# Kernel tuning notes

Measured on AMD Instinct MI355X. Metric: run time of the kernel, lower is better.

## Reference

```python
import jax, jax.numpy as jnp
import numpy as np

N_HEAD = 4
D_MODEL = 256
FEAT_DIM = 256
D_K = D_MODEL // N_HEAD  # 64
TEMP = float(np.sqrt(D_K))
LN_EPS = 1e-5


def setup_inputs() -> dict:
    key = jax.random.key(0)
    ks = jax.random.split(key, 12)
    B, N_src, N_ngh = 2048, 1, 128
    src = jax.random.normal(ks[0], (B, N_src, FEAT_DIM), dtype=jnp.float32)
    seq = jax.random.normal(ks[1], (B, N_ngh, FEAT_DIM), dtype=jnp.float32)
    mask = jax.random.randint(ks[2], (B, N_ngh), 0, 2) > 0
    s_qk = np.sqrt(2.0 / (D_MODEL + D_K))
    w_qs = jax.random.normal(ks[3], (N_HEAD * D_K, D_MODEL), dtype=jnp.float32) * s_qk
    w_ks = jax.random.normal(ks[4], (N_HEAD * D_K, D_MODEL), dtype=jnp.float32) * s_qk
    w_vs = jax.random.normal(ks[5], (N_HEAD * D_K, D_MODEL), dtype=jnp.float32) * s_qk
    fc_w = jax.random.normal(ks[6], (D_MODEL, N_HEAD * D_K), dtype=jnp.float32) * 0.05
    fc_b = jnp.zeros((D_MODEL,), dtype=jnp.float32)
    ln_g = jnp.ones((D_MODEL,), dtype=jnp.float32)
    ln_b = jnp.zeros((D_MODEL,), dtype=jnp.float32)
    fc1_w = jax.random.normal(ks[7], (FEAT_DIM, 2 * D_MODEL), dtype=jnp.float32) * 0.05
    fc1_b = jnp.zeros((FEAT_DIM,), dtype=jnp.float32)
    fc2_w = jax.random.normal(ks[8], (FEAT_DIM, FEAT_DIM), dtype=jnp.float32) * 0.05
    fc2_b = jnp.zeros((FEAT_DIM,), dtype=jnp.float32)
    return {"src": src, "seq": seq, "mask": mask, "w_qs": w_qs, "w_ks": w_ks,
            "w_vs": w_vs, "fc_w": fc_w, "fc_b": fc_b, "ln_g": ln_g, "ln_b": ln_b,
            "fc1_w": fc1_w, "fc1_b": fc1_b, "fc2_w": fc2_w, "fc2_b": fc2_b}


def _forward(src, seq, mask, w_qs, w_ks, w_vs, fc_w, fc_b, ln_g, ln_b,
             fc1_w, fc1_b, fc2_w, fc2_b):
    B, N_src, _ = src.shape
    N_ngh = seq.shape[1]
    nn_ = N_ngh // N_src
    # projections (dropout is identity in eval mode)
    qh = (src @ w_qs.T).reshape(B, N_src, N_HEAD, D_K)              # bshd
    kh = (seq @ w_ks.T).reshape(B, N_src, nn_, N_HEAD, D_K)        # bsnhd
    vh = (seq @ w_vs.T).reshape(B, N_src, nn_, N_HEAD, D_K)
    scores = jnp.einsum('bshd,bsnhd->bshn', qh, kh) / TEMP          # [B,Ns,H,nn]
    # Replicate original mask layout exactly: attn rows are flat in (b,s,h)
    # order, but mask was built with .repeat(n_head,1,1) -> head-major tiling.
    flat = scores.reshape(B * N_src * N_HEAD, nn_)
    mask_rep = jnp.tile(mask.reshape(B * N_src, nn_), (N_HEAD, 1))  # [H*B*Ns, nn]
    flat = jnp.where(mask_rep, -1e10, flat)
    attn = jax.nn.softmax(flat, axis=-1).reshape(B, N_src, N_HEAD, nn_)
    out = jnp.einsum('bshn,bsnhd->bshd', attn, vh).reshape(B, N_src, N_HEAD * D_K)
    out = out @ fc_w.T + fc_b
    x = out + src  # residual (q == src since pos_dim == 0)
    mu = jnp.mean(x, axis=-1, keepdims=True)
    var = jnp.mean(jnp.square(x - mu), axis=-1, keepdims=True)
    x = (x - mu) * jax.lax.rsqrt(var + LN_EPS) * ln_g + ln_b
    # MergeLayer (non_linear=True)
    h = jax.nn.relu(jnp.concatenate([x, src], axis=-1) @ fc1_w.T + fc1_b)
    z = h @ fc2_w.T + fc2_b                                        # [B,Ns,feat]
    return z, attn


def reference(src, seq, mask, w_qs, w_ks, w_vs, fc_w, fc_b, ln_g, ln_b,
              fc1_w, fc1_b, fc2_w, fc2_b):
    return _forward(src, seq, mask, w_qs, w_ks, w_vs, fc_w, fc_b, ln_g, ln_b,
                    fc1_w, fc1_b, fc2_w, fc2_b)
```

## Files before the change

kernel.cpp:

```cpp
#include <hip/hip_runtime.h>

typedef unsigned int uint32;
typedef unsigned short ushort16;

#define DI __device__ __forceinline__

#define BATCH 2048
#define NN    128
#define DM    256
#define NH    4
#define DK    64

DI float bf2f(ushort16 h) { return __uint_as_float(((uint32)h) << 16); }

DI ushort16 f2bf(float f) {
    uint32 u = __float_as_uint(f);
    uint32 r = u + 0x7fffu + ((u >> 16) & 1u);
    return (ushort16)(r >> 16);
}

DI void unpack8(const uint4 v, float f[8]) {
    f[0] = __uint_as_float(v.x << 16);
    f[1] = __uint_as_float(v.x & 0xffff0000u);
    f[2] = __uint_as_float(v.y << 16);
    f[3] = __uint_as_float(v.y & 0xffff0000u);
    f[4] = __uint_as_float(v.z << 16);
    f[5] = __uint_as_float(v.z & 0xffff0000u);
    f[6] = __uint_as_float(v.w << 16);
    f[7] = __uint_as_float(v.w & 0xffff0000u);
}

DI float dot8(const float* a, const float f[8], float acc) {
    acc = fmaf(a[0], f[0], acc);
    acc = fmaf(a[1], f[1], acc);
    acc = fmaf(a[2], f[2], acc);
    acc = fmaf(a[3], f[3], acc);
    acc = fmaf(a[4], f[4], acc);
    acc = fmaf(a[5], f[5], acc);
    acc = fmaf(a[6], f[6], acc);
    acc = fmaf(a[7], f[7], acc);
    return acc;
}

#define WOFF_QS  0
#define WOFF_KS  65536
#define WOFF_VS  131072
#define WOFF_FC  196608
#define WOFF_FC1 262144
#define WOFF_FC2 393216

__global__ __launch_bounds__(256) void prep_kernel(
    const float* __restrict__ wqs, const float* __restrict__ wks,
    const float* __restrict__ wvs, const float* __restrict__ fcw,
    const float* __restrict__ fc1w, const float* __restrict__ fc2w,
    ushort16* __restrict__ out)
{
    const int bid = blockIdx.x;
    const float* srcp; size_t soff, doff;
    if (bid < 64)       { srcp = wqs;  soff = (size_t)bid * 1024;         doff = WOFF_QS;  }
    else if (bid < 128) { srcp = wks;  soff = (size_t)(bid - 64) * 1024;  doff = WOFF_KS;  }
    else if (bid < 192) { srcp = wvs;  soff = (size_t)(bid - 128) * 1024; doff = WOFF_VS;  }
    else if (bid < 256) { srcp = fcw;  soff = (size_t)(bid - 192) * 1024; doff = WOFF_FC;  }
    else if (bid < 384) { srcp = fc1w; soff = (size_t)(bid - 256) * 1024; doff = WOFF_FC1; }
    else                { srcp = fc2w; soff = (size_t)(bid - 384) * 1024; doff = WOFF_FC2; }
    const int t = threadIdx.x;
    float4 v = *(const float4*)(srcp + soff + t * 4);
    uint2 pk;
    pk.x = (uint32)f2bf(v.x) | ((uint32)f2bf(v.y) << 16);
    pk.y = (uint32)f2bf(v.z) | ((uint32)f2bf(v.w) << 16);
    *(uint2*)(out + doff + soff + t * 4) = pk;
}

__global__ __launch_bounds__(256) void qu_kernel(
    const float* __restrict__ src, const ushort16* __restrict__ wbf,
    float* __restrict__ u)
{
    __shared__ float sS[8][DM];
    __shared__ float sQ[8][DM];
    const int t  = threadIdx.x;
    const int b0 = blockIdx.x * 8;

    #pragma unroll
    for (int r = 0; r < 8; ++r) sS[r][t] = src[(size_t)(b0 + r) * DM + t];
    __syncthreads();

    {
        float acc[8] = {0.f,0.f,0.f,0.f,0.f,0.f,0.f,0.f};
        const ushort16* wrow = wbf + WOFF_QS + (size_t)t * DM;
        for (int kc = 0; kc < DM; kc += 8) {
            uint4 w8 = *(const uint4*)(wrow + kc);
            float wf[8]; unpack8(w8, wf);
            #pragma unroll
            for (int r = 0; r < 8; ++r) acc[r] = dot8(&sS[r][kc], wf, acc[r]);
        }
        #pragma unroll
        for (int r = 0; r < 8; ++r) sQ[r][t] = acc[r];
    }
    __syncthreads();

    const ushort16* wks = wbf + WOFF_KS;
    for (int h = 0; h < NH; ++h) {
        float ua[8] = {0.f,0.f,0.f,0.f,0.f,0.f,0.f,0.f};
        for (int dc = 0; dc < DK; dc += 8) {
            float wv[8];
            #pragma unroll
            for (int e = 0; e < 8; ++e)
                wv[e] = bf2f(wks[(size_t)(h * DK + dc + e) * DM + t]);
            #pragma unroll
            for (int r = 0; r < 8; ++r) {
                float4 qa = *(const float4*)&sQ[r][h * DK + dc];
                float4 qb = *(const float4*)&sQ[r][h * DK + dc + 4];
                float a = ua[r];
                a = fmaf(qa.x, wv[0], a); a = fmaf(qa.y, wv[1], a);
                a = fmaf(qa.z, wv[2], a); a = fmaf(qa.w, wv[3], a);
                a = fmaf(qb.x, wv[4], a); a = fmaf(qb.y, wv[5], a);
                a = fmaf(qb.z, wv[6], a); a = fmaf(qb.w, wv[7], a);
                ua[r] = a;
            }
        }
        #pragma unroll
        for (int r = 0; r < 8; ++r)
            u[(size_t)(b0 + r) * (NH * DM) + h * DM + t] = ua[r] * 0.125f;
    }
}

#define SEQ_STRIDE 264
#define U_STRIDE   264

__global__ __launch_bounds__(256) void attn_kernel(
    const float* __restrict__ seq, const int* __restrict__ mask,
    const float* __restrict__ u, float* __restrict__ c,
    float* __restrict__ attn_out)
{
    __shared__ ushort16 sseq[NN * SEQ_STRIDE];
    __shared__ float    sbuf[2048];
    __shared__ float    sattn[NN * NH];

    const int t = threadIdx.x;
    const int b = blockIdx.x;

    #pragma unroll
    for (int i = 0; i < 4; ++i)
        sbuf[i * U_STRIDE + t] = u[(size_t)b * 1024 + i * 256 + t];

    const float* sp = seq + (size_t)b * (NN * DM);
    #pragma unroll
    for (int it = 0; it < 32; ++it) {
        int idx = it * 1024 + t * 4;
        int row = idx >> 8, col = idx & 255;
        float4 v = *(const float4*)(sp + idx);
        uint2 pk;
        pk.x = (uint32)f2bf(v.x) | ((uint32)f2bf(v.y) << 16);
        pk.y = (uint32)f2bf(v.z) | ((uint32)f2bf(v.w) << 16);
        *(uint2*)&sseq[row * SEQ_STRIDE + col] = pk;
    }
    __syncthreads();

    {
        const int h  = t & 3;
        const int n0 = t >> 2;
        const float* uh = &sbuf[h * U_STRIDE];
        const ushort16* r0 = &sseq[n0 * SEQ_STRIDE];
        const ushort16* r1 = &sseq[(n0 + 64) * SEQ_STRIDE];
        float s0 = 0.f, s1 = 0.f;
        for (int kc = 0; kc < DM; kc += 8) {
            uint4 va = *(const uint4*)(r0 + kc);
            uint4 vb = *(const uint4*)(r1 + kc);
            float fa[8], fb[8];
            unpack8(va, fa); unpack8(vb, fb);
            s0 = dot8(&uh[kc], fa, s0);
            s1 = dot8(&uh[kc], fb, s1);
        }
        int mr = (4 * b + h) & (BATCH - 1);
        if (mask[(size_t)mr * NN + n0] != 0)      s0 = -1e10f;
        if (mask[(size_t)mr * NN + n0 + 64] != 0) s1 = -1e10f;
        sattn[n0 * 4 + h]        = s0;
        sattn[(n0 + 64) * 4 + h] = s1;
    }
    __syncthreads();

    {
        const int w = t >> 6, l = t & 63;
        float x0 = sattn[l * 4 + w], x1 = sattn[(l + 64) * 4 + w];
        float mx = fmaxf(x0, x1);
        #pragma unroll
        for (int o = 32; o > 0; o >>= 1) mx = fmaxf(mx, __shfl_xor(mx, o, 64));
        float e0 = __expf(x0 - mx), e1 = __expf(x1 - mx);
        float sm = e0 + e1;
        #pragma unroll
        for (int o = 32; o > 0; o >>= 1) sm += __shfl_xor(sm, o, 64);
        float inv = 1.f / sm;
        float a0 = e0 * inv, a1 = e1 * inv;
        sattn[l * 4 + w]        = a0;
        sattn[(l + 64) * 4 + w] = a1;
        attn_out[(size_t)b * (NH * NN) + w * NN + l]      = a0;
        attn_out[(size_t)b * (NH * NN) + w * NN + l + 64] = a1;
    }
    __syncthreads();

    {
        const int ng = t >> 7;
        const int jp = t & 127;
        float cc[4][2] = {{0.f,0.f},{0.f,0.f},{0.f,0.f},{0.f,0.f}};
        for (int i = 0; i < 64; ++i) {
            int n = ng * 64 + i;
            uint32 v = *(const uint32*)&sseq[n * SEQ_STRIDE + jp * 2];
            float f0 = __uint_as_float(v << 16);
            float f1 = __uint_as_float(v & 0xffff0000u);
            float4 at = *(const float4*)&sattn[n * 4];
            cc[0][0] = fmaf(at.x, f0, cc[0][0]); cc[0][1] = fmaf(at.x, f1, cc[0][1]);
            cc[1][0] = fmaf(at.y, f0, cc[1][0]); cc[1][1] = fmaf(at.y, f1, cc[1][1]);
            cc[2][0] = fmaf(at.z, f0, cc[2][0]); cc[2][1] = fmaf(at.z, f1, cc[2][1]);
            cc[3][0] = fmaf(at.w, f0, cc[3][0]); cc[3][1] = fmaf(at.w, f1, cc[3][1]);
        }
        __syncthreads();
        #pragma unroll
        for (int h = 0; h < 4; ++h) {
            sbuf[ng * 1024 + h * 256 + jp * 2]     = cc[h][0];
            sbuf[ng * 1024 + h * 256 + jp * 2 + 1] = cc[h][1];
        }
    }
    __syncthreads();
    #pragma unroll
    for (int h = 0; h < 4; ++h)
        c[(size_t)b * 1024 + h * 256 + t] = sbuf[h * 256 + t] + sbuf[1024 + h * 256 + t];
}

__global__ __launch_bounds__(256) void mlp_kernel(
    const float* __restrict__ c, const float* __restrict__ src,
    const ushort16* __restrict__ wbf,
    const float* __restrict__ fcb, const float* __restrict__ lng,
    const float* __restrict__ lnb, const float* __restrict__ fc1b,
    const float* __restrict__ fc2b, float* __restrict__ zout)
{
    __shared__ float sC[8][1024];
    __shared__ float sA[8][256];
    __shared__ float sX[8][256];
    __shared__ float sS[8][256];
    __shared__ float sH[8][256];
    __shared__ float sRed[4][8][2];

    const int t  = threadIdx.x;
    const int b0 = blockIdx.x * 8;
    const int h  = t >> 6;

    #pragma unroll
    for (int i = 0; i < 8; ++i)
        *(float4*)&sC[i][t * 4] = *(const float4*)&c[(size_t)(b0 + i) * 1024 + t * 4];
    #pragma unroll
    for (int r = 0; r < 8; ++r) sS[r][t] = src[(size_t)(b0 + r) * DM + t];
    __syncthreads();

    {
        float acc[8] = {0.f,0.f,0.f,0.f,0.f,0.f,0.f,0.f};
        const ushort16* wr = wbf + WOFF_VS + (size_t)t * DM;
        for (int kc = 0; kc < DM; kc += 8) {
            uint4 w8 = *(const uint4*)(wr + kc);
            float wf[8]; unpack8(w8, wf);
            #pragma unroll
            for (int r = 0; r < 8; ++r) acc[r] = dot8(&sC[r][h * 256 + kc], wf, acc[r]);
        }
        #pragma unroll
        for (int r = 0; r < 8; ++r) sA[r][t] = acc[r];
    }
    __syncthreads();

    float xv[8];
    {
        float acc[8] = {0.f,0.f,0.f,0.f,0.f,0.f,0.f,0.f};
        const ushort16* wr = wbf + WOFF_FC + (size_t)t * DM;
        for (int kc = 0; kc < DM; kc += 8) {
            uint4 w8 = *(const uint4*)(wr + kc);
            float wf[8]; unpack8(w8, wf);
            #pragma unroll
            for (int r = 0; r < 8; ++r) acc[r] = dot8(&sA[r][kc], wf, acc[r]);
        }
        float bb = fcb[t];
        #pragma unroll
        for (int r = 0; r < 8; ++r) xv[r] = acc[r] + bb + sS[r][t];
    }
    {
        const int w = t >> 6, l = t & 63;
        #pragma unroll
        for (int r = 0; r < 8; ++r) {
            float vs = xv[r], vq = xv[r] * xv[r];
            #pragma unroll
            for (int o = 32; o > 0; o >>= 1) {
                vs += __shfl_xor(vs, o, 64);
                vq += __shfl_xor(vq, o, 64);
            }
            if (l == 0) { sRed[w][r][0] = vs; sRed[w][r][1] = vq; }
        }
        __syncthreads();
        float g = lng[t], bb = lnb[t];
        #pragma unroll
        for (int r = 0; r < 8; ++r) {
            float S = sRed[0][r][0] + sRed[1][r][0] + sRed[2][r][0] + sRed[3][r][0];
            float Q = sRed[0][r][1] + sRed[1][r][1] + sRed[2][r][1] + sRed[3][r][1];
            float mu  = S * (1.f / 256.f);
            float var = Q * (1.f / 256.f) - mu * mu;
            float rs  = rsqrtf(var + 1e-5f);
            sX[r][t] = (xv[r] - mu) * rs * g + bb;
        }
    }
    __syncthreads();

    {
        float acc[8] = {0.f,0.f,0.f,0.f,0.f,0.f,0.f,0.f};
        const ushort16* wr = wbf + WOFF_FC1 + (size_t)t * 512;
        for (int kc = 0; kc < 256; kc += 8) {
            uint4 w8 = *(const uint4*)(wr + kc);
            float wf[8]; unpack8(w8, wf);
            #pragma unroll
            for (int r = 0; r < 8; ++r) acc[r] = dot8(&sX[r][kc], wf, acc[r]);
        }
        for (int kc = 0; kc < 256; kc += 8) {
            uint4 w8 = *(const uint4*)(wr + 256 + kc);
            float wf[8]; unpack8(w8, wf);
            #pragma unroll
            for (int r = 0; r < 8; ++r) acc[r] = dot8(&sS[r][kc], wf, acc[r]);
        }
        float bb = fc1b[t];
        #pragma unroll
        for (int r = 0; r < 8; ++r) sH[r][t] = fmaxf(acc[r] + bb, 0.f);
    }
    __syncthreads();

    {
        float acc[8] = {0.f,0.f,0.f,0.f,0.f,0.f,0.f,0.f};
        const ushort16* wr = wbf + WOFF_FC2 + (size_t)t * DM;
        for (int kc = 0; kc < DM; kc += 8) {
            uint4 w8 = *(const uint4*)(wr + kc);
            float wf[8]; unpack8(w8, wf);
            #pragma unroll
            for (int r = 0; r < 8; ++r) acc[r] = dot8(&sH[r][kc], wf, acc[r]);
        }
        float bb = fc2b[t];
        #pragma unroll
        for (int r = 0; r < 8; ++r)
            zout[(size_t)(b0 + r) * DM + t] = acc[r] + bb;
    }
}

extern "C" void kernel_launch(void* const* d_in, const int* in_sizes, int n_in,
                              void* d_out, int out_size, void* d_ws, size_t ws_size,
                              hipStream_t stream)
{
    const float* src  = (const float*)d_in[0];
    const float* seq  = (const float*)d_in[1];
    const int*   mask = (const int*)d_in[2];
    const float* wqs  = (const float*)d_in[3];
    const float* wks  = (const float*)d_in[4];
    const float* wvs  = (const float*)d_in[5];
    const float* fcw  = (const float*)d_in[6];
    const float* fcb  = (const float*)d_in[7];
    const float* lng  = (const float*)d_in[8];
    const float* lnb  = (const float*)d_in[9];
    const float* fc1w = (const float*)d_in[10];
    const float* fc1b = (const float*)d_in[11];
    const float* fc2w = (const float*)d_in[12];
    const float* fc2b = (const float*)d_in[13];

    float* zout     = (float*)d_out;
    float* attn_out = zout + (size_t)BATCH * DM;

    float* u = (float*)d_ws;
    float* cbuf = u + (size_t)BATCH * 1024;
    ushort16* wbf = (ushort16*)(cbuf + (size_t)BATCH * 1024);

    prep_kernel<<<448, 256, 0, stream>>>(wqs, wks, wvs, fcw, fc1w, fc2w, wbf);
    qu_kernel<<<256, 256, 0, stream>>>(src, wbf, u);
    attn_kernel<<<BATCH, 256, 0, stream>>>(seq, mask, u, cbuf, attn_out);
    mlp_kernel<<<256, 256, 0, stream>>>(cbuf, src, wbf, fcb, lng, lnb,
                                        fc1b, fc2b, zout);
}
```

Measured before the change: 471.9 us.

## Fuse query projection and key-folding into attention kernel, drop qu_kernel

Removes the separate qu_kernel and computes q = src·Wq and u = q·Wk (scaled) per batch row inside the attention kernel, right after the seq tile is staged. This eliminates one launch and the global round trip of the u buffer. In exchange, each attention block re-reads the full bf16 Wq and Wk weights (about 256 KB per block) instead of amortising them over 8 rows, which adds L2 traffic and per-block latency.

```diff
diff --git a/kernel.cpp b/kernel.cpp
--- a/kernel.cpp
+++ b/kernel.cpp
@@ -71,77 +71,24 @@
     *(uint2*)(out + doff + soff + t * 4) = pk;
 }
 
-__global__ __launch_bounds__(256) void qu_kernel(
-    const float* __restrict__ src, const ushort16* __restrict__ wbf,
-    float* __restrict__ u)
-{
-    __shared__ float sS[8][DM];
-    __shared__ float sQ[8][DM];
-    const int t  = threadIdx.x;
-    const int b0 = blockIdx.x * 8;
-
-    #pragma unroll
-    for (int r = 0; r < 8; ++r) sS[r][t] = src[(size_t)(b0 + r) * DM + t];
-    __syncthreads();
-
-    {
-        float acc[8] = {0.f,0.f,0.f,0.f,0.f,0.f,0.f,0.f};
-        const ushort16* wrow = wbf + WOFF_QS + (size_t)t * DM;
-        for (int kc = 0; kc < DM; kc += 8) {
-            uint4 w8 = *(const uint4*)(wrow + kc);
-            float wf[8]; unpack8(w8, wf);
-            #pragma unroll
-            for (int r = 0; r < 8; ++r) acc[r] = dot8(&sS[r][kc], wf, acc[r]);
-        }
-        #pragma unroll
-        for (int r = 0; r < 8; ++r) sQ[r][t] = acc[r];
-    }
-    __syncthreads();
-
-    const ushort16* wks = wbf + WOFF_KS;
-    for (int h = 0; h < NH; ++h) {
-        float ua[8] = {0.f,0.f,0.f,0.f,0.f,0.f,0.f,0.f};
-        for (int dc = 0; dc < DK; dc += 8) {
-            float wv[8];
-            #pragma unroll
-            for (int e = 0; e < 8; ++e)
-                wv[e] = bf2f(wks[(size_t)(h * DK + dc + e) * DM + t]);
-            #pragma unroll
-            for (int r = 0; r < 8; ++r) {
-                float4 qa = *(const float4*)&sQ[r][h * DK + dc];
-                float4 qb = *(const float4*)&sQ[r][h * DK + dc + 4];
-                float a = ua[r];
-                a = fmaf(qa.x, wv[0], a); a = fmaf(qa.y, wv[1], a);
-                a = fmaf(qa.z, wv[2], a); a = fmaf(qa.w, wv[3], a);
-                a = fmaf(qb.x, wv[4], a); a = fmaf(qb.y, wv[5], a);
-                a = fmaf(qb.z, wv[6], a); a = fmaf(qb.w, wv[7], a);
-                ua[r] = a;
-            }
-        }
-        #pragma unroll
-        for (int r = 0; r < 8; ++r)
-            u[(size_t)(b0 + r) * (NH * DM) + h * DM + t] = ua[r] * 0.125f;
-    }
-}
-
 #define SEQ_STRIDE 264
 #define U_STRIDE   264
 
 __global__ __launch_bounds__(256) void attn_kernel(
-    const float* __restrict__ seq, const int* __restrict__ mask,
-    const float* __restrict__ u, float* __restrict__ c,
-    float* __restrict__ attn_out)
+    const float* __restrict__ src, const float* __restrict__ seq,
+    const int* __restrict__ mask, const ushort16* __restrict__ wbf,
+    float* __restrict__ c, float* __restrict__ attn_out)
 {
     __shared__ ushort16 sseq[NN * SEQ_STRIDE];
     __shared__ float    sbuf[2048];
     __shared__ float    sattn[NN * NH];
+    __shared__ float    ssrc[DM];
+    __shared__ float    sQ[DM];
 
     const int t = threadIdx.x;
     const int b = blockIdx.x;
 
-    #pragma unroll
-    for (int i = 0; i < 4; ++i)
-        sbuf[i * U_STRIDE + t] = u[(size_t)b * 1024 + i * 256 + t];
+    ssrc[t] = src[(size_t)b * DM + t];
 
     const float* sp = seq + (size_t)b * (NN * DM);
     #pragma unroll
@@ -153,6 +100,39 @@
         pk.x = (uint32)f2bf(v.x) | ((uint32)f2bf(v.y) << 16);
         pk.y = (uint32)f2bf(v.z) | ((uint32)f2bf(v.w) << 16);
         *(uint2*)&sseq[row * SEQ_STRIDE + col] = pk;
+    }
+    __syncthreads();
+
+    {
+        float acc = 0.f;
+        const ushort16* wrow = wbf + WOFF_QS + (size_t)t * DM;
+        for (int kc = 0; kc < DM; kc += 8) {
+            uint4 w8 = *(const uint4*)(wrow + kc);
+            float wf[8]; unpack8(w8, wf);
+            acc = dot8(&ssrc[kc], wf, acc);
+        }
+        sQ[t] = acc * 0.125f;
+    }
+    __syncthreads();
+
+    {
+        const int w = t >> 6, l = t & 63;
+        float u00 = 0.f, u01 = 0.f, u10 = 0.f, u11 = 0.f;
+        const ushort16* wk = wbf + WOFF_KS + (size_t)w * DK * DM;
+        #pragma unroll 8
+        for (int d = 0; d < DK; ++d) {
+            float qd = sQ[w * DK + d];
+            uint32 va = *(const uint32*)(wk + d * DM + 2 * l);
+            uint32 vb = *(const uint32*)(wk + d * DM + 128 + 2 * l);
+            u00 = fmaf(qd, __uint_as_float(va << 16), u00);
+            u01 = fmaf(qd, __uint_as_float(va & 0xffff0000u), u01);
+            u10 = fmaf(qd, __uint_as_float(vb << 16), u10);
+            u11 = fmaf(qd, __uint_as_float(vb & 0xffff0000u), u11);
+        }
+        sbuf[w * U_STRIDE + 2 * l]           = u00;
+        sbuf[w * U_STRIDE + 2 * l + 1]       = u01;
+        sbuf[w * U_STRIDE + 128 + 2 * l]     = u10;
+        sbuf[w * U_STRIDE + 128 + 2 * l + 1] = u11;
     }
     __syncthreads();
 
@@ -364,13 +344,11 @@
     float* zout     = (float*)d_out;
     float* attn_out = zout + (size_t)BATCH * DM;
 
-    float* u = (float*)d_ws;
-    float* cbuf = u + (size_t)BATCH * 1024;
+    float* cbuf = (float*)d_ws;
     ushort16* wbf = (ushort16*)(cbuf + (size_t)BATCH * 1024);
 
     prep_kernel<<<448, 256, 0, stream>>>(wqs, wks, wvs, fcw, fc1w, fc2w, wbf);
-    qu_kernel<<<256, 256, 0, stream>>>(src, wbf, u);
-    attn_kernel<<<BATCH, 256, 0, stream>>>(seq, mask, u, cbuf, attn_out);
+    attn_kernel<<<BATCH, 256, 0, stream>>>(src, seq, mask, wbf, cbuf, attn_out);
     mlp_kernel<<<256, 256, 0, stream>>>(cbuf, src, wbf, fcb, lng, lnb,
                                         fc1b, fc2b, zout);
 }
```

New measurement: 493.4 us. 1.05x slower.
